# Kernel tuning notes

Measured on AMD Instinct MI355X. Metric: run time of the kernel, lower is better.

The kernel has to match this reference:

```python
import jax, jax.numpy as jnp
import numpy as np


def setup_inputs() -> dict:
    key = jax.random.key(0)
    k1, k2, k3, k4 = jax.random.split(key, 4)
    B, L, R, H, D = 64, 512, 512, 512, 256
    return {
        "lstm_lt": jax.random.normal(k1, (B, L, H), dtype=jnp.float32),
        "lstm_rt": jax.random.normal(k2, (B, R, H), dtype=jnp.float32),
        "atten_W": jax.random.normal(k3, (H, D), dtype=jnp.float32) * 0.05,
        "diagnoal_W": jax.random.normal(k4, (1, 1, D), dtype=jnp.float32) * 0.05,
    }


def reference(lstm_lt, lstm_rt, atten_W, diagnoal_W):
    # Projection (the original's broadcast-multiply-sum is exactly a GEMM):
    # atten_lt[b,l,d] = tanh(sum_h lstm_lt[b,l,h] * W[h,d]) * diag_W[d]
    atten_lt = jnp.tanh(jnp.einsum('blh,hd->bld', lstm_lt, atten_W)) * diagnoal_W
    atten_rt = jnp.tanh(jnp.einsum('brh,hd->brd', lstm_rt, atten_W))
    # batch_dot over the attention dim -> (B, L, R)
    atten_value = jnp.einsum('bld,brd->blr', atten_lt, atten_rt)
    # No masks supplied (len(inputs)==2 path); softmax over last axis.
    return jax.nn.softmax(atten_value, axis=-1)
```

## Files before the change

### kernel.cpp

```cpp
#include <hip/hip_runtime.h>

typedef __attribute__((ext_vector_type(8))) __bf16 bf16x8;
typedef __attribute__((ext_vector_type(4))) float f32x4;

#define DI __device__ __forceinline__

DI unsigned short f2bf(float x) {
  unsigned u = __float_as_uint(x);
  u += 0x7fffu + ((u >> 16) & 1u);
  return (unsigned short)(u >> 16);
}

DI bf16x8 cvt8(f32x4 lo, f32x4 hi) {
  bf16x8 r;
  r[0] = (__bf16)lo.x; r[1] = (__bf16)lo.y; r[2] = (__bf16)lo.z; r[3] = (__bf16)lo.w;
  r[4] = (__bf16)hi.x; r[5] = (__bf16)hi.y; r[6] = (__bf16)hi.z; r[7] = (__bf16)hi.w;
  return r;
}

DI float tanh_fast(float x) {
  float ax = fabsf(x);
  float e = __expf(-2.0f * ax);
  float t = (1.0f - e) / (1.0f + e);
  return x < 0.0f ? -t : t;
}

DI void glds16(const void* gptr, void* lptr) {
  __builtin_amdgcn_global_load_lds(
      (const __attribute__((address_space(1))) unsigned int*)gptr,
      (__attribute__((address_space(3))) unsigned int*)lptr, 16, 0, 0);
}

__global__ void k_wt(const float* __restrict__ W, unsigned short* __restrict__ Wt) {
  int n = blockIdx.x;
  int t = threadIdx.x;
  int k = t * 4;
  ushort4 v;
  v.x = f2bf(W[(k + 0) * 256 + n]);
  v.y = f2bf(W[(k + 1) * 256 + n]);
  v.z = f2bf(W[(k + 2) * 256 + n]);
  v.w = f2bf(W[(k + 3) * 256 + n]);
  *(ushort4*)&Wt[n * 512 + k] = v;
}

__global__ __launch_bounds__(512, 4) void k_proj(
    const float* __restrict__ Alt, const float* __restrict__ Art,
    const unsigned short* __restrict__ Wt, const float* __restrict__ diag,
    unsigned short* __restrict__ Olt, unsigned short* __restrict__ Ort) {
  __shared__ __align__(16) float As[128 * 64];
  __shared__ __align__(16) unsigned short Bs[256 * 64];

  int bx = blockIdx.x;
  bool is_lt = bx < 256;
  int m0 = (is_lt ? bx : bx - 256) * 128;
  const char* Abase = (const char*)((is_lt ? Alt : Art) + (size_t)m0 * 512);
  unsigned short* O = (is_lt ? Olt : Ort) + (size_t)m0 * 256;

  int tid  = threadIdx.x;
  int lane = tid & 63;
  int wid  = tid >> 6;
  int wm   = wid >> 2;
  int wn   = wid & 3;
  int l15  = lane & 15;
  int quad = lane >> 4;
  int r7   = l15 & 7;

  int lr4 = lane >> 4, c16 = lane & 15;
  int aoff = lr4 * 2048 + ((c16 ^ lr4) << 4);
  int lr8 = lane >> 3, s8 = lane & 7;
  int boff = lr8 * 1024 + ((s8 ^ lr8) << 4);

  const char* Bbase = (const char*)Wt;
  char* AsB = (char*)As;
  char* BsB = (char*)Bs;

  f32x4 zero = {0.0f, 0.0f, 0.0f, 0.0f};
  f32x4 acc[4][4];
#pragma unroll
  for (int i = 0; i < 4; i++)
#pragma unroll
    for (int j = 0; j < 4; j++) acc[i][j] = zero;

  for (int k0 = 0; k0 < 512; k0 += 64) {
#pragma unroll
    for (int i = 0; i < 4; i++) {
      int j = wid * 4 + i;
      glds16(Abase + (size_t)j * 8192 + (size_t)k0 * 4 + (aoff ^ ((j & 1) << 6)),
             AsB + j * 1024);
    }
#pragma unroll
    for (int i = 0; i < 4; i++) {
      int j = wid * 4 + i;
      glds16(Bbase + (size_t)j * 8192 + (size_t)k0 * 2 + boff, BsB + j * 1024);
    }
    __syncthreads();

#pragma unroll
    for (int ks = 0; ks < 2; ks++) {
      bf16x8 a[4], b[4];
#pragma unroll
      for (int mt = 0; mt < 4; mt++) {
        int row = wm * 64 + mt * 16 + l15;
        int c0 = ks * 8 + quad * 2;
        f32x4 lo = *(const f32x4*)(AsB + row * 256 + (((c0    ) ^ r7) << 4));
        f32x4 hi = *(const f32x4*)(AsB + row * 256 + (((c0 + 1) ^ r7) << 4));
        a[mt] = cvt8(lo, hi);
      }
#pragma unroll
      for (int nt = 0; nt < 4; nt++) {
        int row = wn * 64 + nt * 16 + l15;
        int c = ks * 4 + quad;
        b[nt] = *(const bf16x8*)(BsB + row * 128 + ((c ^ r7) << 4));
      }
#pragma unroll
      for (int mt = 0; mt < 4; mt++)
#pragma unroll
        for (int nt = 0; nt < 4; nt++)
          acc[mt][nt] = __builtin_amdgcn_mfma_f32_16x16x32_bf16(a[mt], b[nt], acc[mt][nt], 0, 0, 0);
    }
    __syncthreads();
  }

  float dscale[4];
#pragma unroll
  for (int nt = 0; nt < 4; nt++)
    dscale[nt] = is_lt ? diag[wn * 64 + nt * 16 + l15] : 1.0f;

#pragma unroll
  for (int mt = 0; mt < 4; mt++) {
#pragma unroll
    for (int r = 0; r < 4; r++) {
      int row = wm * 64 + mt * 16 + quad * 4 + r;
#pragma unroll
      for (int nt = 0; nt < 4; nt++) {
        int col = wn * 64 + nt * 16 + l15;
        O[(size_t)row * 256 + col] = f2bf(tanh_fast(acc[mt][nt][r]) * dscale[nt]);
      }
    }
  }
}

__global__ __launch_bounds__(512, 4) void k_attn(
    const unsigned short* __restrict__ Lt, const unsigned short* __restrict__ Rt,
    float* __restrict__ Out) {
  __shared__ __align__(16) unsigned short Ls[64 * 64];
  __shared__ __align__(16) unsigned short Rs[512 * 64];
  __shared__ float red[8][64];
  __shared__ float rowv[64];

  int bx = blockIdx.x;
  int b  = (bx & 7) * 8 + ((bx >> 3) & 7);
  int l0 = (bx >> 6) * 64;
  const char* Lb = (const char*)(Lt + ((size_t)b * 512 + l0) * 256);
  const char* Rb = (const char*)(Rt + (size_t)b * 512 * 256);
  float* Ob = Out + ((size_t)b * 512 + l0) * 512;

  int tid  = threadIdx.x;
  int lane = tid & 63;
  int wid  = tid >> 6;
  int l15  = lane & 15;
  int quad = lane >> 4;
  int r7   = l15 & 7;

  int lr8 = lane >> 3, s8 = lane & 7;
  int goff = lr8 * 512 + ((s8 ^ lr8) << 4);

  char* LsB = (char*)Ls;
  char* RsB = (char*)Rs;

  f32x4 zero = {0.0f, 0.0f, 0.0f, 0.0f};
  f32x4 acc[4][4];
#pragma unroll
  for (int i = 0; i < 4; i++)
#pragma unroll
    for (int j = 0; j < 4; j++) acc[i][j] = zero;

  for (int k0 = 0; k0 < 256; k0 += 64) {
    glds16(Lb + (size_t)wid * 4096 + (size_t)k0 * 2 + goff, LsB + wid * 1024);
#pragma unroll
    for (int i = 0; i < 8; i++) {
      int j = wid * 8 + i;
      glds16(Rb + (size_t)j * 4096 + (size_t)k0 * 2 + goff, RsB + j * 1024);
    }
    __syncthreads();

#pragma unroll
    for (int ks = 0; ks < 2; ks++) {
      bf16x8 a[4], bb[4];
#pragma unroll
      for (int mt = 0; mt < 4; mt++) {
        int row = mt * 16 + l15;
        int c = ks * 4 + quad;
        a[mt] = *(const bf16x8*)(LsB + row * 128 + ((c ^ r7) << 4));
      }
#pragma unroll
      for (int nt = 0; nt < 4; nt++) {
        int row = wid * 64 + nt * 16 + l15;
        int c = ks * 4 + quad;
        bb[nt] = *(const bf16x8*)(RsB + row * 128 + ((c ^ r7) << 4));
      }
#pragma unroll
      for (int mt = 0; mt < 4; mt++)
#pragma unroll
        for (int nt = 0; nt < 4; nt++)
          acc[mt][nt] = __builtin_amdgcn_mfma_f32_16x16x32_bf16(a[mt], bb[nt], acc[mt][nt], 0, 0, 0);
    }
    __syncthreads();
  }

#pragma unroll
  for (int mt = 0; mt < 4; mt++) {
#pragma unroll
    for (int r = 0; r < 4; r++) {
      float m = fmaxf(fmaxf(acc[mt][0][r], acc[mt][1][r]),
                      fmaxf(acc[mt][2][r], acc[mt][3][r]));
      m = fmaxf(m, __shfl_xor(m, 1));
      m = fmaxf(m, __shfl_xor(m, 2));
      m = fmaxf(m, __shfl_xor(m, 4));
      m = fmaxf(m, __shfl_xor(m, 8));
      if (l15 == 0) red[wid][mt * 16 + quad * 4 + r] = m;
    }
  }
  __syncthreads();
  if (tid < 64) {
    float m = red[0][tid];
#pragma unroll
    for (int w = 1; w < 8; w++) m = fmaxf(m, red[w][tid]);
    rowv[tid] = m;
  }
  __syncthreads();

#pragma unroll
  for (int mt = 0; mt < 4; mt++) {
#pragma unroll
    for (int r = 0; r < 4; r++) {
      float base = rowv[mt * 16 + quad * 4 + r];
      float s = 0.0f;
#pragma unroll
      for (int nt = 0; nt < 4; nt++) {
        float e = __expf(acc[mt][nt][r] - base);
        acc[mt][nt][r] = e;
        s += e;
      }
      s += __shfl_xor(s, 1);
      s += __shfl_xor(s, 2);
      s += __shfl_xor(s, 4);
      s += __shfl_xor(s, 8);
      if (l15 == 0) red[wid][mt * 16 + quad * 4 + r] = s;
    }
  }
  __syncthreads();
  if (tid < 64) {
    float s = red[0][tid];
#pragma unroll
    for (int w = 1; w < 8; w++) s += red[w][tid];
    rowv[tid] = 1.0f / s;
  }
  __syncthreads();

#pragma unroll
  for (int mt = 0; mt < 4; mt++) {
#pragma unroll
    for (int r = 0; r < 4; r++) {
      int row = mt * 16 + quad * 4 + r;
      float inv = rowv[row];
#pragma unroll
      for (int nt = 0; nt < 4; nt++) {
        int col = wid * 64 + nt * 16 + l15;
        Ob[(size_t)row * 512 + col] = acc[mt][nt][r] * inv;
      }
    }
  }
}

extern "C" void kernel_launch(void* const* d_in, const int* in_sizes, int n_in,
                              void* d_out, int out_size, void* d_ws, size_t ws_size,
                              hipStream_t stream) {
  const float* lstm_lt = (const float*)d_in[0];
  const float* lstm_rt = (const float*)d_in[1];
  const float* W       = (const float*)d_in[2];
  const float* diag    = (const float*)d_in[3];
  float* out = (float*)d_out;

  unsigned short* Wt  = (unsigned short*)d_ws;
  unsigned short* Olt = (unsigned short*)((char*)d_ws + (size_t)256 * 512 * 2);
  unsigned short* Ort = Olt + (size_t)32768 * 256;

  k_wt<<<dim3(256), dim3(128), 0, stream>>>(W, Wt);
  k_proj<<<dim3(512), dim3(512), 0, stream>>>(lstm_lt, lstm_rt, Wt, diag, Olt, Ort);
  k_attn<<<dim3(512), dim3(512), 0, stream>>>(Olt, Ort, out);
}
```

Measured before the change: 212.8 us.

## Double-buffer LDS tiles in projection and attention GEMMs with async prefetch

Both GEMM kernels now use two LDS buffers and issue the global_load_lds for the next K tile before the MFMA work on the current tile. A custom wait (vmcnt(0) plus s_barrier) replaces the per-iteration __syncthreads pairs, and s_setprio raises wave priority around the MFMA bursts. This aims to hide global-load latency behind matrix math. The cost is double the LDS footprint and launch bounds lowered from 4 to 2, which cuts resident blocks per CU and leaves fewer waves to hide latency.

```diff
diff --git a/kernel.cpp b/kernel.cpp
--- a/kernel.cpp
+++ b/kernel.cpp
@@ -29,6 +29,13 @@
   __builtin_amdgcn_global_load_lds(
       (const __attribute__((address_space(1))) unsigned int*)gptr,
       (__attribute__((address_space(3))) unsigned int*)lptr, 16, 0, 0);
+}
+
+DI void pipewait() {
+  __builtin_amdgcn_sched_barrier(0);
+  asm volatile("s_waitcnt vmcnt(0)" ::: "memory");
+  __builtin_amdgcn_s_barrier();
+  __builtin_amdgcn_sched_barrier(0);
 }
 
 __global__ void k_wt(const float* __restrict__ W, unsigned short* __restrict__ Wt) {
@@ -43,12 +50,12 @@
   *(ushort4*)&Wt[n * 512 + k] = v;
 }
 
-__global__ __launch_bounds__(512, 4) void k_proj(
+__global__ __launch_bounds__(512, 2) void k_proj(
     const float* __restrict__ Alt, const float* __restrict__ Art,
     const unsigned short* __restrict__ Wt, const float* __restrict__ diag,
     unsigned short* __restrict__ Olt, unsigned short* __restrict__ Ort) {
-  __shared__ __align__(16) float As[128 * 64];
-  __shared__ __align__(16) unsigned short Bs[256 * 64];
+  __shared__ __align__(16) float As[2][128 * 64];
+  __shared__ __align__(16) unsigned short Bs[2][256 * 64];
 
   int bx = blockIdx.x;
   bool is_lt = bx < 256;
@@ -71,8 +78,6 @@
   int boff = lr8 * 1024 + ((s8 ^ lr8) << 4);
 
   const char* Bbase = (const char*)Wt;
-  char* AsB = (char*)As;
-  char* BsB = (char*)Bs;
 
   f32x4 zero = {0.0f, 0.0f, 0.0f, 0.0f};
   f32x4 acc[4][4];
@@ -81,20 +86,21 @@
 #pragma unroll
     for (int j = 0; j < 4; j++) acc[i][j] = zero;
 
-  for (int k0 = 0; k0 < 512; k0 += 64) {
+  auto stage = [&](int buf, int k0) {
+    char* AsB = (char*)&As[buf][0];
+    char* BsB = (char*)&Bs[buf][0];
 #pragma unroll
     for (int i = 0; i < 4; i++) {
       int j = wid * 4 + i;
       glds16(Abase + (size_t)j * 8192 + (size_t)k0 * 4 + (aoff ^ ((j & 1) << 6)),
              AsB + j * 1024);
-    }
-#pragma unroll
-    for (int i = 0; i < 4; i++) {
-      int j = wid * 4 + i;
       glds16(Bbase + (size_t)j * 8192 + (size_t)k0 * 2 + boff, BsB + j * 1024);
     }
-    __syncthreads();
-
+  };
+
+  auto compute = [&](int buf) {
+    const char* AsB = (const char*)&As[buf][0];
+    const char* BsB = (const char*)&Bs[buf][0];
 #pragma unroll
     for (int ks = 0; ks < 2; ks++) {
       bf16x8 a[4], b[4];
@@ -112,13 +118,26 @@
         int c = ks * 4 + quad;
         b[nt] = *(const bf16x8*)(BsB + row * 128 + ((c ^ r7) << 4));
       }
+      __builtin_amdgcn_s_setprio(1);
 #pragma unroll
       for (int mt = 0; mt < 4; mt++)
 #pragma unroll
         for (int nt = 0; nt < 4; nt++)
           acc[mt][nt] = __builtin_amdgcn_mfma_f32_16x16x32_bf16(a[mt], b[nt], acc[mt][nt], 0, 0, 0);
-    }
-    __syncthreads();
+      __builtin_amdgcn_s_setprio(0);
+    }
+  };
+
+  stage(0, 0);
+  pipewait();
+
+  for (int k0 = 0; k0 < 512; k0 += 128) {
+    stage(1, k0 + 64);
+    compute(0);
+    pipewait();
+    if (k0 + 128 < 512) stage(0, k0 + 128);
+    compute(1);
+    if (k0 + 128 < 512) pipewait();
   }
 
   float dscale[4];
@@ -140,11 +159,11 @@
   }
 }
 
-__global__ __launch_bounds__(512, 4) void k_attn(
+__global__ __launch_bounds__(512, 2) void k_attn(
     const unsigned short* __restrict__ Lt, const unsigned short* __restrict__ Rt,
     float* __restrict__ Out) {
-  __shared__ __align__(16) unsigned short Ls[64 * 64];
-  __shared__ __align__(16) unsigned short Rs[512 * 64];
+  __shared__ __align__(16) unsigned short Ls[2][64 * 64];
+  __shared__ __align__(16) unsigned short Rs[2][512 * 64];
   __shared__ float red[8][64];
   __shared__ float rowv[64];
 
@@ -165,9 +184,6 @@
   int lr8 = lane >> 3, s8 = lane & 7;
   int goff = lr8 * 512 + ((s8 ^ lr8) << 4);
 
-  char* LsB = (char*)Ls;
-  char* RsB = (char*)Rs;
-
   f32x4 zero = {0.0f, 0.0f, 0.0f, 0.0f};
   f32x4 acc[4][4];
 #pragma unroll
@@ -175,15 +191,20 @@
 #pragma unroll
     for (int j = 0; j < 4; j++) acc[i][j] = zero;
 
-  for (int k0 = 0; k0 < 256; k0 += 64) {
+  auto stage = [&](int buf, int k0) {
+    char* LsB = (char*)&Ls[buf][0];
+    char* RsB = (char*)&Rs[buf][0];
     glds16(Lb + (size_t)wid * 4096 + (size_t)k0 * 2 + goff, LsB + wid * 1024);
 #pragma unroll
     for (int i = 0; i < 8; i++) {
       int j = wid * 8 + i;
       glds16(Rb + (size_t)j * 4096 + (size_t)k0 * 2 + goff, RsB + j * 1024);
     }
-    __syncthreads();
-
+  };
+
+  auto compute = [&](int buf) {
+    const char* LsB = (const char*)&Ls[buf][0];
+    const char* RsB = (const char*)&Rs[buf][0];
 #pragma unroll
     for (int ks = 0; ks < 2; ks++) {
       bf16x8 a[4], bb[4];
@@ -199,13 +220,25 @@
         int c = ks * 4 + quad;
         bb[nt] = *(const bf16x8*)(RsB + row * 128 + ((c ^ r7) << 4));
       }
+      __builtin_amdgcn_s_setprio(1);
 #pragma unroll
       for (int mt = 0; mt < 4; mt++)
 #pragma unroll
         for (int nt = 0; nt < 4; nt++)
           acc[mt][nt] = __builtin_amdgcn_mfma_f32_16x16x32_bf16(a[mt], bb[nt], acc[mt][nt], 0, 0, 0);
-    }
-    __syncthreads();
+      __builtin_amdgcn_s_setprio(0);
+    }
+  };
+
+  stage(0, 0);
+  pipewait();
+  for (int k0 = 0; k0 < 256; k0 += 128) {
+    stage(1, k0 + 64);
+    compute(0);
+    pipewait();
+    if (k0 + 128 < 256) stage(0, k0 + 128);
+    compute(1);
+    if (k0 + 128 < 256) pipewait();
   }
 
 #pragma unroll
```

After: 220.6 us. 3.7% more time.

## Register-prefetch software pipeline for projection and attention GEMMs, larger proj tile

Applied to the files above, without the earlier changes.

Replaces direct global-to-LDS loads with a register-staged double-buffer pipeline in both GEMM kernels: the next K-slice is loaded into registers during compute and written to LDS between barriers. The projection kernel doubles its M tile to 256 rows, converts A to bf16 once when writing LDS instead of on every fragment read, and halves its grid. The attention kernel keeps the whole L tile resident in LDS with smaller R slices. MFMA sections are raised in priority with setprio. The cost is higher register pressure, with launch bounds lowered to 2 blocks per CU, and fewer blocks in the projection grid.

```diff
diff --git a/kernel.cpp b/kernel.cpp
--- a/kernel.cpp
+++ b/kernel.cpp
@@ -25,10 +25,16 @@
   return x < 0.0f ? -t : t;
 }
 
-DI void glds16(const void* gptr, void* lptr) {
-  __builtin_amdgcn_global_load_lds(
-      (const __attribute__((address_space(1))) unsigned int*)gptr,
-      (__attribute__((address_space(3))) unsigned int*)lptr, 16, 0, 0);
+DI void barx() {
+  __builtin_amdgcn_sched_barrier(0);
+  __builtin_amdgcn_s_barrier();
+  __builtin_amdgcn_sched_barrier(0);
+}
+
+DI void lgkm0() {
+  __builtin_amdgcn_sched_barrier(0);
+  asm volatile("s_waitcnt lgkmcnt(0)" ::: "memory");
+  __builtin_amdgcn_sched_barrier(0);
 }
 
 __global__ void k_wt(const float* __restrict__ W, unsigned short* __restrict__ Wt) {
@@ -43,18 +49,19 @@
   *(ushort4*)&Wt[n * 512 + k] = v;
 }
 
-__global__ __launch_bounds__(512, 4) void k_proj(
+__global__ __launch_bounds__(512, 2) void k_proj(
     const float* __restrict__ Alt, const float* __restrict__ Art,
     const unsigned short* __restrict__ Wt, const float* __restrict__ diag,
     unsigned short* __restrict__ Olt, unsigned short* __restrict__ Ort) {
-  __shared__ __align__(16) float As[128 * 64];
+  __shared__ __align__(16) unsigned short As[256 * 64];
   __shared__ __align__(16) unsigned short Bs[256 * 64];
 
   int bx = blockIdx.x;
-  bool is_lt = bx < 256;
-  int m0 = (is_lt ? bx : bx - 256) * 128;
+  bool is_lt = bx < 128;
+  int m0 = (is_lt ? bx : bx - 128) * 256;
   const char* Abase = (const char*)((is_lt ? Alt : Art) + (size_t)m0 * 512);
   unsigned short* O = (is_lt ? Olt : Ort) + (size_t)m0 * 256;
+  const char* Bbase = (const char*)Wt;
 
   int tid  = threadIdx.x;
   int lane = tid & 63;
@@ -65,46 +72,49 @@
   int quad = lane >> 4;
   int r7   = l15 & 7;
 
-  int lr4 = lane >> 4, c16 = lane & 15;
-  int aoff = lr4 * 2048 + ((c16 ^ lr4) << 4);
-  int lr8 = lane >> 3, s8 = lane & 7;
-  int boff = lr8 * 1024 + ((s8 ^ lr8) << 4);
-
-  const char* Bbase = (const char*)Wt;
+  int srow = wid * 32 + (lane >> 3);
+  int sc   = lane & 7;
+  int wch  = ((sc ^ (lane >> 3)) << 4);
+
   char* AsB = (char*)As;
   char* BsB = (char*)Bs;
 
   f32x4 zero = {0.0f, 0.0f, 0.0f, 0.0f};
-  f32x4 acc[4][4];
-#pragma unroll
-  for (int i = 0; i < 4; i++)
+  f32x4 acc[8][4];
+#pragma unroll
+  for (int i = 0; i < 8; i++)
 #pragma unroll
     for (int j = 0; j < 4; j++) acc[i][j] = zero;
 
-  for (int k0 = 0; k0 < 512; k0 += 64) {
-#pragma unroll
-    for (int i = 0; i < 4; i++) {
-      int j = wid * 4 + i;
-      glds16(Abase + (size_t)j * 8192 + (size_t)k0 * 4 + (aoff ^ ((j & 1) << 6)),
-             AsB + j * 1024);
-    }
-#pragma unroll
-    for (int i = 0; i < 4; i++) {
-      int j = wid * 4 + i;
-      glds16(Bbase + (size_t)j * 8192 + (size_t)k0 * 2 + boff, BsB + j * 1024);
-    }
-    __syncthreads();
-
+  f32x4 aLo[4], aHi[4];
+  uint4 bR[4];
+
+  auto issue = [&](int t) {
+#pragma unroll
+    for (int j = 0; j < 4; j++) {
+      const char* ap = Abase + (size_t)(srow + j * 8) * 2048 + t * 256 + sc * 32;
+      aLo[j] = *(const f32x4*)(ap);
+      aHi[j] = *(const f32x4*)(ap + 16);
+      bR[j]  = *(const uint4*)(Bbase + (size_t)(srow + j * 8) * 1024 + t * 128 + sc * 16);
+    }
+  };
+  auto writeS = [&]() {
+#pragma unroll
+    for (int j = 0; j < 4; j++) {
+      int r = srow + j * 8;
+      *(bf16x8*)(AsB + r * 128 + wch) = cvt8(aLo[j], aHi[j]);
+      *(uint4*)(BsB + r * 128 + wch) = bR[j];
+    }
+  };
+  auto compute = [&]() {
 #pragma unroll
     for (int ks = 0; ks < 2; ks++) {
-      bf16x8 a[4], b[4];
-#pragma unroll
-      for (int mt = 0; mt < 4; mt++) {
-        int row = wm * 64 + mt * 16 + l15;
-        int c0 = ks * 8 + quad * 2;
-        f32x4 lo = *(const f32x4*)(AsB + row * 256 + (((c0    ) ^ r7) << 4));
-        f32x4 hi = *(const f32x4*)(AsB + row * 256 + (((c0 + 1) ^ r7) << 4));
-        a[mt] = cvt8(lo, hi);
+      bf16x8 a[8], b[4];
+#pragma unroll
+      for (int mt = 0; mt < 8; mt++) {
+        int row = wm * 128 + mt * 16 + l15;
+        int c = ks * 4 + quad;
+        a[mt] = *(const bf16x8*)(AsB + row * 128 + ((c ^ r7) << 4));
       }
 #pragma unroll
       for (int nt = 0; nt < 4; nt++) {
@@ -112,13 +122,31 @@
         int c = ks * 4 + quad;
         b[nt] = *(const bf16x8*)(BsB + row * 128 + ((c ^ r7) << 4));
       }
-#pragma unroll
-      for (int mt = 0; mt < 4; mt++)
+      __builtin_amdgcn_s_setprio(1);
+#pragma unroll
+      for (int mt = 0; mt < 8; mt++)
 #pragma unroll
         for (int nt = 0; nt < 4; nt++)
           acc[mt][nt] = __builtin_amdgcn_mfma_f32_16x16x32_bf16(a[mt], b[nt], acc[mt][nt], 0, 0, 0);
-    }
-    __syncthreads();
+      __builtin_amdgcn_s_setprio(0);
+    }
+  };
+
+  issue(0);
+  writeS();
+  issue(1);
+  lgkm0();
+  barx();
+
+  for (int t = 0; t < 8; t++) {
+    compute();
+    if (t < 7) {
+      barx();
+      writeS();
+      if (t < 6) issue(t + 2);
+      lgkm0();
+      barx();
+    }
   }
 
   float dscale[4];
@@ -127,10 +155,10 @@
     dscale[nt] = is_lt ? diag[wn * 64 + nt * 16 + l15] : 1.0f;
 
 #pragma unroll
-  for (int mt = 0; mt < 4; mt++) {
+  for (int mt = 0; mt < 8; mt++) {
 #pragma unroll
     for (int r = 0; r < 4; r++) {
-      int row = wm * 64 + mt * 16 + quad * 4 + r;
+      int row = wm * 128 + mt * 16 + quad * 4 + r;
 #pragma unroll
       for (int nt = 0; nt < 4; nt++) {
         int col = wn * 64 + nt * 16 + l15;
@@ -140,11 +168,11 @@
   }
 }
 
-__global__ __launch_bounds__(512, 4) void k_attn(
+__global__ __launch_bounds__(512, 2) void k_attn(
     const unsigned short* __restrict__ Lt, const unsigned short* __restrict__ Rt,
     float* __restrict__ Out) {
-  __shared__ __align__(16) unsigned short Ls[64 * 64];
-  __shared__ __align__(16) unsigned short Rs[512 * 64];
+  __shared__ __align__(16) unsigned short Ls[64 * 256];
+  __shared__ __align__(16) unsigned short Rs[512 * 32];
   __shared__ float red[8][64];
   __shared__ float rowv[64];
 
@@ -161,9 +189,8 @@
   int l15  = lane & 15;
   int quad = lane >> 4;
   int r7   = l15 & 7;
-
-  int lr8 = lane >> 3, s8 = lane & 7;
-  int goff = lr8 * 512 + ((s8 ^ lr8) << 4);
+  int swb  = (l15 >> 1) & 3;
+  int swr  = (tid >> 1) & 3;
 
   char* LsB = (char*)Ls;
   char* RsB = (char*)Rs;
@@ -175,37 +202,64 @@
 #pragma unroll
     for (int j = 0; j < 4; j++) acc[i][j] = zero;
 
-  for (int k0 = 0; k0 < 256; k0 += 64) {
-    glds16(Lb + (size_t)wid * 4096 + (size_t)k0 * 2 + goff, LsB + wid * 1024);
-#pragma unroll
-    for (int i = 0; i < 8; i++) {
-      int j = wid * 8 + i;
-      glds16(Rb + (size_t)j * 4096 + (size_t)k0 * 2 + goff, RsB + j * 1024);
-    }
-    __syncthreads();
-
-#pragma unroll
-    for (int ks = 0; ks < 2; ks++) {
-      bf16x8 a[4], bb[4];
-#pragma unroll
-      for (int mt = 0; mt < 4; mt++) {
-        int row = mt * 16 + l15;
-        int c = ks * 4 + quad;
-        a[mt] = *(const bf16x8*)(LsB + row * 128 + ((c ^ r7) << 4));
-      }
-#pragma unroll
-      for (int nt = 0; nt < 4; nt++) {
-        int row = wid * 64 + nt * 16 + l15;
-        int c = ks * 4 + quad;
-        bb[nt] = *(const bf16x8*)(RsB + row * 128 + ((c ^ r7) << 4));
-      }
-#pragma unroll
-      for (int mt = 0; mt < 4; mt++)
-#pragma unroll
-        for (int nt = 0; nt < 4; nt++)
-          acc[mt][nt] = __builtin_amdgcn_mfma_f32_16x16x32_bf16(a[mt], bb[nt], acc[mt][nt], 0, 0, 0);
-    }
-    __syncthreads();
+  uint4 rR[4];
+  auto issueR = [&](int t) {
+#pragma unroll
+    for (int j = 0; j < 4; j++)
+      rR[j] = *(const uint4*)(Rb + (size_t)tid * 512 + t * 64 + j * 16);
+  };
+  auto writeR = [&]() {
+#pragma unroll
+    for (int j = 0; j < 4; j++)
+      *(uint4*)(RsB + tid * 64 + ((j ^ swr) << 4)) = rR[j];
+  };
+
+  {
+    int rowL = tid >> 3, cL = tid & 7;
+    uint4 lL[4];
+#pragma unroll
+    for (int j = 0; j < 4; j++)
+      lL[j] = *(const uint4*)(Lb + (size_t)rowL * 512 + cL * 64 + j * 16);
+#pragma unroll
+    for (int j = 0; j < 4; j++) {
+      int ch = cL * 4 + j;
+      *(uint4*)(LsB + rowL * 512 + ((ch ^ (rowL & 7)) << 4)) = lL[j];
+    }
+  }
+  issueR(0);
+  writeR();
+  issueR(1);
+  lgkm0();
+  barx();
+
+  for (int t = 0; t < 8; t++) {
+    bf16x8 a[4], bb[4];
+#pragma unroll
+    for (int mt = 0; mt < 4; mt++) {
+      int row = mt * 16 + l15;
+      int c = t * 4 + quad;
+      a[mt] = *(const bf16x8*)(LsB + row * 512 + ((c ^ r7) << 4));
+    }
+#pragma unroll
+    for (int nt = 0; nt < 4; nt++) {
+      int row = wid * 64 + nt * 16 + l15;
+      bb[nt] = *(const bf16x8*)(RsB + row * 64 + ((quad ^ swb) << 4));
+    }
+    __builtin_amdgcn_s_setprio(1);
+#pragma unroll
+    for (int mt = 0; mt < 4; mt++)
+#pragma unroll
+      for (int nt = 0; nt < 4; nt++)
+        acc[mt][nt] = __builtin_amdgcn_mfma_f32_16x16x32_bf16(a[mt], bb[nt], acc[mt][nt], 0, 0, 0);
+    __builtin_amdgcn_s_setprio(0);
+
+    if (t < 7) {
+      barx();
+      writeR();
+      if (t < 6) issueR(t + 2);
+      lgkm0();
+      barx();
+    }
   }
 
 #pragma unroll
@@ -287,6 +341,6 @@
   unsigned short* Ort = Olt + (size_t)32768 * 256;
 
   k_wt<<<dim3(256), dim3(128), 0, stream>>>(W, Wt);
-  k_proj<<<dim3(512), dim3(512), 0, stream>>>(lstm_lt, lstm_rt, Wt, diag, Olt, Ort);
+  k_proj<<<dim3(256), dim3(512), 0, stream>>>(lstm_lt, lstm_rt, Wt, diag, Olt, Ort);
   k_attn<<<dim3(512), dim3(512), 0, stream>>>(Olt, Ort, out);
 }
```

Result: slower. 252.8 us (+18.8%).

## Pre-swizzle B operands into MFMA fragment layout and load them directly to registers

Applied to the files above, without the earlier changes.

W^T and the right projection are written in a layout where each 1KB chunk is exactly one 16x32 MFMA B-fragment. Both GEMM kernels can then load B operands straight from global memory into registers with coalesced 16-byte loads, with no LDS staging. k_attn also loads the whole 64x256 left tile once and drops the per-k-step barriers. s_setprio is added around the MFMA bursts. This cuts LDS traffic and synchronisation, but B-operand latency is now exposed to global/L2 and the right projection is written with scattered 2-byte stores.

```diff
diff --git a/kernel.cpp b/kernel.cpp
--- a/kernel.cpp
+++ b/kernel.cpp
@@ -31,16 +31,20 @@
       (__attribute__((address_space(3))) unsigned int*)lptr, 16, 0, 0);
 }
 
+
 __global__ void k_wt(const float* __restrict__ W, unsigned short* __restrict__ Wt) {
-  int n = blockIdx.x;
-  int t = threadIdx.x;
-  int k = t * 4;
-  ushort4 v;
-  v.x = f2bf(W[(k + 0) * 256 + n]);
-  v.y = f2bf(W[(k + 1) * 256 + n]);
-  v.z = f2bf(W[(k + 2) * 256 + n]);
-  v.w = f2bf(W[(k + 3) * 256 + n]);
-  *(ushort4*)&Wt[n * 512 + k] = v;
+  int n  = blockIdx.x;
+  int k8 = threadIdx.x;
+  unsigned v[8];
+#pragma unroll
+  for (int j = 0; j < 8; j++) v[j] = f2bf(W[(k8 * 8 + j) * 256 + n]);
+  uint4 p;
+  p.x = v[0] | (v[1] << 16);
+  p.y = v[2] | (v[3] << 16);
+  p.z = v[4] | (v[5] << 16);
+  p.w = v[6] | (v[7] << 16);
+  size_t idx = ((size_t)(n >> 4) * 16 + (k8 >> 2)) * 512 + (k8 & 3) * 128 + (n & 15) * 8;
+  *(uint4*)&Wt[idx] = p;
 }
 
 __global__ __launch_bounds__(512, 4) void k_proj(
@@ -48,13 +52,12 @@
     const unsigned short* __restrict__ Wt, const float* __restrict__ diag,
     unsigned short* __restrict__ Olt, unsigned short* __restrict__ Ort) {
   __shared__ __align__(16) float As[128 * 64];
-  __shared__ __align__(16) unsigned short Bs[256 * 64];
 
   int bx = blockIdx.x;
   bool is_lt = bx < 256;
   int m0 = (is_lt ? bx : bx - 256) * 128;
   const char* Abase = (const char*)((is_lt ? Alt : Art) + (size_t)m0 * 512);
-  unsigned short* O = (is_lt ? Olt : Ort) + (size_t)m0 * 256;
+  const char* Bt = (const char*)Wt;
 
   int tid  = threadIdx.x;
   int lane = tid & 63;
@@ -67,12 +70,8 @@
 
   int lr4 = lane >> 4, c16 = lane & 15;
   int aoff = lr4 * 2048 + ((c16 ^ lr4) << 4);
-  int lr8 = lane >> 3, s8 = lane & 7;
-  int boff = lr8 * 1024 + ((s8 ^ lr8) << 4);
-
-  const char* Bbase = (const char*)Wt;
+
   char* AsB = (char*)As;
-  char* BsB = (char*)Bs;
 
   f32x4 zero = {0.0f, 0.0f, 0.0f, 0.0f};
   f32x4 acc[4][4];
@@ -82,22 +81,25 @@
     for (int j = 0; j < 4; j++) acc[i][j] = zero;
 
   for (int k0 = 0; k0 < 512; k0 += 64) {
+    uint4 bv[2][4];
+#pragma unroll
+    for (int ks = 0; ks < 2; ks++)
+#pragma unroll
+      for (int nt = 0; nt < 4; nt++)
+        bv[ks][nt] = *(const uint4*)(
+            Bt + (((size_t)(wn * 4 + nt) * 16 + (k0 >> 5) + ks) << 10) + lane * 16);
+
 #pragma unroll
     for (int i = 0; i < 4; i++) {
       int j = wid * 4 + i;
       glds16(Abase + (size_t)j * 8192 + (size_t)k0 * 4 + (aoff ^ ((j & 1) << 6)),
              AsB + j * 1024);
     }
-#pragma unroll
-    for (int i = 0; i < 4; i++) {
-      int j = wid * 4 + i;
-      glds16(Bbase + (size_t)j * 8192 + (size_t)k0 * 2 + boff, BsB + j * 1024);
-    }
     __syncthreads();
 
 #pragma unroll
     for (int ks = 0; ks < 2; ks++) {
-      bf16x8 a[4], b[4];
+      bf16x8 a[4];
 #pragma unroll
       for (int mt = 0; mt < 4; mt++) {
         int row = wm * 64 + mt * 16 + l15;
@@ -106,17 +108,14 @@
         f32x4 hi = *(const f32x4*)(AsB + row * 256 + (((c0 + 1) ^ r7) << 4));
         a[mt] = cvt8(lo, hi);
       }
-#pragma unroll
-      for (int nt = 0; nt < 4; nt++) {
-        int row = wn * 64 + nt * 16 + l15;
-        int c = ks * 4 + quad;
-        b[nt] = *(const bf16x8*)(BsB + row * 128 + ((c ^ r7) << 4));
-      }
+      __builtin_amdgcn_s_setprio(1);
 #pragma unroll
       for (int mt = 0; mt < 4; mt++)
 #pragma unroll
         for (int nt = 0; nt < 4; nt++)
-          acc[mt][nt] = __builtin_amdgcn_mfma_f32_16x16x32_bf16(a[mt], b[nt], acc[mt][nt], 0, 0, 0);
+          acc[mt][nt] = __builtin_amdgcn_mfma_f32_16x16x32_bf16(
+              a[mt], __builtin_bit_cast(bf16x8, bv[ks][nt]), acc[mt][nt], 0, 0, 0);
+      __builtin_amdgcn_s_setprio(0);
     }
     __syncthreads();
   }
@@ -126,25 +125,43 @@
   for (int nt = 0; nt < 4; nt++)
     dscale[nt] = is_lt ? diag[wn * 64 + nt * 16 + l15] : 1.0f;
 
-#pragma unroll
-  for (int mt = 0; mt < 4; mt++) {
-#pragma unroll
-    for (int r = 0; r < 4; r++) {
-      int row = wm * 64 + mt * 16 + quad * 4 + r;
-#pragma unroll
-      for (int nt = 0; nt < 4; nt++) {
-        int col = wn * 64 + nt * 16 + l15;
-        O[(size_t)row * 256 + col] = f2bf(tanh_fast(acc[mt][nt][r]) * dscale[nt]);
-      }
-    }
+  if (is_lt) {
+    unsigned short* O = Olt + (size_t)m0 * 256;
+#pragma unroll
+    for (int mt = 0; mt < 4; mt++)
+#pragma unroll
+      for (int r = 0; r < 4; r++) {
+        int row = wm * 64 + mt * 16 + quad * 4 + r;
+#pragma unroll
+        for (int nt = 0; nt < 4; nt++) {
+          int col = wn * 64 + nt * 16 + l15;
+          O[(size_t)row * 256 + col] = f2bf(tanh_fast(acc[mt][nt][r]) * dscale[nt]);
+        }
+      }
+  } else {
+#pragma unroll
+    for (int mt = 0; mt < 4; mt++)
+#pragma unroll
+      for (int r = 0; r < 4; r++) {
+        int row = wm * 64 + mt * 16 + quad * 4 + r;
+        int m = m0 + row;
+        int bb = m >> 9, rr = m & 511;
+#pragma unroll
+        for (int nt = 0; nt < 4; nt++) {
+          int d = wn * 64 + nt * 16 + l15;
+          size_t idx = (size_t)bb * 131072 +
+                       ((size_t)(rr >> 4) * 8 + (d >> 5)) * 512 +
+                       ((d >> 3) & 3) * 128 + (rr & 15) * 8 + (d & 7);
+          Ort[idx] = f2bf(tanh_fast(acc[mt][nt][r]));
+        }
+      }
   }
 }
 
 __global__ __launch_bounds__(512, 4) void k_attn(
     const unsigned short* __restrict__ Lt, const unsigned short* __restrict__ Rt,
     float* __restrict__ Out) {
-  __shared__ __align__(16) unsigned short Ls[64 * 64];
-  __shared__ __align__(16) unsigned short Rs[512 * 64];
+  __shared__ __align__(16) unsigned short Ls[64 * 256];
   __shared__ float red[8][64];
   __shared__ float rowv[64];
 
@@ -152,7 +169,7 @@
   int b  = (bx & 7) * 8 + ((bx >> 3) & 7);
   int l0 = (bx >> 6) * 64;
   const char* Lb = (const char*)(Lt + ((size_t)b * 512 + l0) * 256);
-  const char* Rb = (const char*)(Rt + (size_t)b * 512 * 256);
+  const char* Rb = (const char*)Rt + (size_t)b * 262144;
   float* Ob = Out + ((size_t)b * 512 + l0) * 512;
 
   int tid  = threadIdx.x;
@@ -162,11 +179,7 @@
   int quad = lane >> 4;
   int r7   = l15 & 7;
 
-  int lr8 = lane >> 3, s8 = lane & 7;
-  int goff = lr8 * 512 + ((s8 ^ lr8) << 4);
-
   char* LsB = (char*)Ls;
-  char* RsB = (char*)Rs;
 
   f32x4 zero = {0.0f, 0.0f, 0.0f, 0.0f};
   f32x4 acc[4][4];
@@ -175,37 +188,34 @@
 #pragma unroll
     for (int j = 0; j < 4; j++) acc[i][j] = zero;
 
-  for (int k0 = 0; k0 < 256; k0 += 64) {
-    glds16(Lb + (size_t)wid * 4096 + (size_t)k0 * 2 + goff, LsB + wid * 1024);
-#pragma unroll
-    for (int i = 0; i < 8; i++) {
-      int j = wid * 8 + i;
-      glds16(Rb + (size_t)j * 4096 + (size_t)k0 * 2 + goff, RsB + j * 1024);
-    }
-    __syncthreads();
-
-#pragma unroll
-    for (int ks = 0; ks < 2; ks++) {
-      bf16x8 a[4], bb[4];
-#pragma unroll
-      for (int mt = 0; mt < 4; mt++) {
-        int row = mt * 16 + l15;
-        int c = ks * 4 + quad;
-        a[mt] = *(const bf16x8*)(LsB + row * 128 + ((c ^ r7) << 4));
-      }
-#pragma unroll
-      for (int nt = 0; nt < 4; nt++) {
-        int row = wid * 64 + nt * 16 + l15;
-        int c = ks * 4 + quad;
-        bb[nt] = *(const bf16x8*)(RsB + row * 128 + ((c ^ r7) << 4));
-      }
-#pragma unroll
-      for (int mt = 0; mt < 4; mt++)
-#pragma unroll
-        for (int nt = 0; nt < 4; nt++)
-          acc[mt][nt] = __builtin_amdgcn_mfma_f32_16x16x32_bf16(a[mt], bb[nt], acc[mt][nt], 0, 0, 0);
-    }
-    __syncthreads();
+#pragma unroll
+  for (int i = 0; i < 4; i++) {
+    int grow = wid * 8 + i * 2 + (lane >> 5);
+    glds16(Lb + (size_t)grow * 512 + (((lane & 31) ^ (grow & 7)) << 4),
+           LsB + (wid * 8 + i * 2) * 512 + (lane & 31) * 16 + (lane >> 5) * 512);
+  }
+  __syncthreads();
+
+  for (int t = 0; t < 8; t++) {
+    uint4 rv[4];
+#pragma unroll
+    for (int nt = 0; nt < 4; nt++)
+      rv[nt] = *(const uint4*)(
+          Rb + (((size_t)(wid * 4 + nt) * 8 + t) << 10) + lane * 16);
+    bf16x8 a[4];
+#pragma unroll
+    for (int mt = 0; mt < 4; mt++) {
+      int row = mt * 16 + l15;
+      a[mt] = *(const bf16x8*)(LsB + row * 512 + (((t * 4 + quad) ^ r7) << 4));
+    }
+    __builtin_amdgcn_s_setprio(1);
+#pragma unroll
+    for (int mt = 0; mt < 4; mt++)
+#pragma unroll
+      for (int nt = 0; nt < 4; nt++)
+        acc[mt][nt] = __builtin_amdgcn_mfma_f32_16x16x32_bf16(
+            a[mt], __builtin_bit_cast(bf16x8, rv[nt]), acc[mt][nt], 0, 0, 0);
+    __builtin_amdgcn_s_setprio(0);
   }
 
 #pragma unroll
@@ -286,7 +296,7 @@
   unsigned short* Olt = (unsigned short*)((char*)d_ws + (size_t)256 * 512 * 2);
   unsigned short* Ort = Olt + (size_t)32768 * 256;
 
-  k_wt<<<dim3(256), dim3(128), 0, stream>>>(W, Wt);
+  k_wt<<<dim3(256), dim3(64), 0, stream>>>(W, Wt);
   k_proj<<<dim3(512), dim3(512), 0, stream>>>(lstm_lt, lstm_rt, Wt, diag, Olt, Ort);
   k_attn<<<dim3(512), dim3(512), 0, stream>>>(Olt, Ort, out);
 }
```

Measured after the change: 217.1 us. 2.0% more time.
